# Kernel optimization log

Hardware: AMD Instinct MI355X
Metric: run time of the kernel (lower is better)

The kernel has to match this reference:

```python
import jax, jax.numpy as jnp
import numpy as np

B, M, T, H = 32, 2048, 8, 64  # batch, measurements, num_tags, hidden_dim
LATENT, TRIL = 3, 6
NEG_INF = -1e9  # masked-out logit value for segment softmax


def _linear_init(key, fan_in, fan_out):
    # torch nn.Linear default: U(-1/sqrt(fan_in), 1/sqrt(fan_in)) for W and b
    bound = 1.0 / np.sqrt(fan_in)
    kw, kb = jax.random.split(key)
    w = jax.random.uniform(kw, (fan_in, fan_out), minval=-bound, maxval=bound, dtype=jnp.float32)
    b = jax.random.uniform(kb, (fan_out,), minval=-bound, maxval=bound, dtype=jnp.float32)
    return w, b


def setup_inputs() -> dict:
    key = jax.random.key(0)
    ks = jax.random.split(key, 14)
    inp = {}
    inp['measurements'] = jax.random.normal(ks[0], (B, M, 5), dtype=jnp.float32)
    inp['measurement_to_tag_mapping'] = jax.random.randint(ks[1], (B, M), 0, T, dtype=jnp.int32)
    inp['me_w1'], inp['me_b1'] = _linear_init(ks[2], 5, H)
    inp['me_w2'], inp['me_b2'] = _linear_init(ks[3], H, H)
    inp['q_w'], inp['q_b'] = _linear_init(ks[4], H, H)
    inp['k_w'], inp['k_b'] = _linear_init(ks[5], H, H)
    inp['v_w'], inp['v_b'] = _linear_init(ks[6], H, H)
    inp['a1_w1'], inp['a1_b1'] = _linear_init(ks[7], H, H // 2)
    inp['a1_w2'], inp['a1_b2'] = _linear_init(ks[8], H // 2, 1)
    inp['a2_w1'], inp['a2_b1'] = _linear_init(ks[9], H, H // 2)
    inp['a2_w2'], inp['a2_b2'] = _linear_init(ks[10], H // 2, 1)
    inp['mu_w'], inp['mu_b'] = _linear_init(ks[11], H, LATENT)
    inp['logL_w'], inp['logL_b'] = _linear_init(ks[12], H, TRIL)
    return inp


def reference(measurements, measurement_to_tag_mapping,
              me_w1, me_b1, me_w2, me_b2,
              q_w, q_b, k_w, k_b, v_w, v_b,
              a1_w1, a1_b1, a1_w2, a1_b2,
              a2_w1, a2_b1, a2_w2, a2_b2,
              mu_w, mu_b, logL_w, logL_b):
    # measurement encoder: two Linear+ReLU layers -> [B, M, H]
    feat = jax.nn.relu(measurements @ me_w1 + me_b1)
    feat = jax.nn.relu(feat @ me_w2 + me_b2)

    # self-attention with residual
    q = feat @ q_w + q_b
    k = feat @ k_w + k_b
    v = feat @ v_w + v_b
    scale = jnp.sqrt(jnp.float32(H))
    scores = jnp.einsum('bmh,bnh->bmn', q, k) / scale  # [B, M, M]
    feat = feat + jnp.einsum('bmn,bnh->bmh', jax.nn.softmax(scores, axis=-1), v)

    # per-measurement attention logits (attention_net1) -> [B, M]
    a1 = (jax.nn.relu(feat @ a1_w1 + a1_b1) @ a1_w2 + a1_b2)[..., 0]

    # segment softmax per tag id: mask [B, M, T]
    tag_mask = measurement_to_tag_mapping[..., None] == jnp.arange(T)
    seg_logits = jnp.where(tag_mask, a1[..., None], NEG_INF)
    seg_w = jax.nn.softmax(seg_logits, axis=1)  # softmax over measurements within each tag
    tag_feat = jnp.einsum('bmt,bmh->bth', seg_w, feat)  # [B, T, H]

    # aggregate tags (attention_net2) -> pose feature [B, H]
    a2 = (jax.nn.relu(tag_feat @ a2_w1 + a2_b1) @ a2_w2 + a2_b2)[..., 0]  # [B, T]
    tag_w = jax.nn.softmax(a2, axis=-1)
    pose = jnp.einsum('bt,bth->bh', tag_w, tag_feat)

    mu = pose @ mu_w + mu_b
    logL = pose @ logL_w + logL_b
    return mu, logL
```

## Files before the change

kernel.cpp:

```cpp
#include <hip/hip_runtime.h>
#include <hip/hip_bf16.h>
#include <cstdint>
#include <cstddef>


typedef short s16x8 __attribute__((ext_vector_type(8)));
typedef float f32x4 __attribute__((ext_vector_type(4)));
typedef float f32x16 __attribute__((ext_vector_type(16)));

#define LOG2E  1.4426950408889634f
#define QSCALE 0.18033688011112042f

__device__ __forceinline__ unsigned short f2bf(float f) {
    unsigned u = __builtin_bit_cast(unsigned, f);
    u += 0x7fffu + ((u >> 16) & 1u);
    return (unsigned short)(u >> 16);
}

__device__ __forceinline__ unsigned cvtpk(float lo, float hi) {
    unsigned r;
    asm("v_cvt_pk_bf16_f32 %0, %1, %2" : "=v"(r) : "v"(lo), "v"(hi));
    return r;
}

__device__ __forceinline__ float exp2_raw(float x) {
    float r;
    asm("v_exp_f32 %0, %1" : "=v"(r) : "v"(x));
    return r;
}

#define PLSWAP(a, b) asm("v_permlane32_swap_b32 %0, %1" : "+v"(a), "+v"(b))

__device__ __forceinline__ void gload_lds16(const void* g, void* l) {
    __builtin_amdgcn_global_load_lds((const __attribute__((address_space(1))) void*)g,
                                     (__attribute__((address_space(3))) void*)l, 16, 0, 0);
}

#define MFMA16(a, b, c) __builtin_amdgcn_mfma_f32_16x16x32_bf16((a), (b), (c), 0, 0, 0)
#define MFMA32(a, b, c) __builtin_amdgcn_mfma_f32_32x32x16_bf16((a), (b), (c), 0, 0, 0)

__global__ void k_prep(const float* __restrict__ w2, const float* __restrict__ qw,
                       const float* __restrict__ kw, const float* __restrict__ vw,
                       const float* __restrict__ a1w1,
                       unsigned short* __restrict__ wt, float* __restrict__ a1w1t)
{
    int tid = threadIdx.x;
    for (int idx = tid; idx < 4096; idx += 256) {
        int o = idx >> 6, i = idx & 63;
        wt[idx]         = f2bf(w2[i * 64 + o]);
        wt[4096 + idx]  = f2bf(qw[i * 64 + o] * QSCALE);
        wt[8192 + idx]  = f2bf(kw[i * 64 + o]);
        wt[12288 + idx] = f2bf(vw[i * 64 + o]);
    }
    for (int idx = tid; idx < 2048; idx += 256) {
        int j = idx >> 6, d = idx & 63;
        a1w1t[idx] = a1w1[d * 32 + j];
    }
}

__global__ __launch_bounds__(256)
void k_encode(const float* __restrict__ meas, const float* __restrict__ w1,
              const float* __restrict__ b1, const float* __restrict__ b2,
              const float* __restrict__ qb, const float* __restrict__ kb,
              const float* __restrict__ vb,
              const unsigned short* __restrict__ wt,
              float* __restrict__ feat,
              unsigned short* __restrict__ qbf, unsigned short* __restrict__ kbf,
              unsigned short* __restrict__ vt)
{
    __shared__ __align__(16) unsigned short hbuf[4][1152];
    int tid = threadIdx.x;
    int w = tid >> 6, lane = tid & 63;
    int g = lane >> 4, c16 = lane & 15;
    int m0 = (blockIdx.x * 4 + w) * 16;
    int b  = m0 >> 11;
    unsigned short* hb = hbuf[w];
    int vrow = lane >> 2, vseg = lane & 3;

    float x[5];
    const float* xr = meas + (size_t)(m0 + c16) * 5;
#pragma unroll
    for (int i = 0; i < 5; ++i) x[i] = xr[i];
    s16x8 aH[2];
#pragma unroll
    for (int s = 0; s < 2; ++s) {
#pragma unroll
        for (int jj = 0; jj < 8; ++jj) {
            int j = 8 * g + jj + 32 * s;
            float acc = b1[j];
#pragma unroll
            for (int i = 0; i < 5; ++i) acc += x[i] * w1[i * 64 + j];
            aH[s][jj] = (short)f2bf(fmaxf(acc, 0.f));
        }
    }

    const f32x4 zero = {0.f, 0.f, 0.f, 0.f};
    f32x4 c[4];

#pragma unroll
    for (int dt = 0; dt < 4; ++dt) {
        c[dt] = zero;
#pragma unroll
        for (int s = 0; s < 2; ++s) {
            s16x8 bf = *(const s16x8*)(wt + (c16 + 16 * dt) * 64 + 32 * s + 8 * g);
            c[dt] = MFMA16(aH[s], bf, c[dt]);
        }
    }
#pragma unroll
    for (int dt = 0; dt < 4; ++dt) {
        int d = c16 + 16 * dt;
        float bias = b2[d];
#pragma unroll
        for (int r = 0; r < 4; ++r) {
            float v = fmaxf(c[dt][r] + bias, 0.f);
            feat[(size_t)(m0 + 4 * g + r) * 64 + d] = v;
            hb[(4 * g + r) * 72 + d] = f2bf(v);
        }
    }
    s16x8 aF[2];
#pragma unroll
    for (int s = 0; s < 2; ++s)
        aF[s] = *(const s16x8*)(hb + c16 * 72 + 32 * s + 8 * g);

    auto gemmW = [&](const unsigned short* wmat, f32x4* cc) {
#pragma unroll
        for (int dt = 0; dt < 4; ++dt) {
            cc[dt] = zero;
#pragma unroll
            for (int s = 0; s < 2; ++s) {
                s16x8 bf = *(const s16x8*)(wmat + (c16 + 16 * dt) * 64 + 32 * s + 8 * g);
                cc[dt] = MFMA16(aF[s], bf, cc[dt]);
            }
        }
    };
    auto storeV = [&](const float* bias4, unsigned short* dstbase) {
#pragma unroll
        for (int dt = 0; dt < 4; ++dt) {
            int d = c16 + 16 * dt;
#pragma unroll
            for (int r = 0; r < 4; ++r)
                hb[(4 * g + r) * 72 + d] = f2bf(c[dt][r] + bias4[dt]);
        }
        s16x8 o0 = *(const s16x8*)(hb + vrow * 72 + vseg * 16);
        s16x8 o1 = *(const s16x8*)(hb + vrow * 72 + vseg * 16 + 8);
        unsigned short* dst = dstbase + (size_t)(m0 + vrow) * 64 + vseg * 16;
        *(s16x8*)dst = o0;
        *(s16x8*)(dst + 8) = o1;
    };

    float bias4[4];
    gemmW(wt + 4096, c);
#pragma unroll
    for (int dt = 0; dt < 4; ++dt) bias4[dt] = qb[c16 + 16 * dt] * QSCALE;
    storeV(bias4, qbf);
    gemmW(wt + 8192, c);
#pragma unroll
    for (int dt = 0; dt < 4; ++dt) bias4[dt] = kb[c16 + 16 * dt];
    storeV(bias4, kbf);
    gemmW(wt + 12288, c);
#pragma unroll
    for (int dt = 0; dt < 4; ++dt) {
        int d = c16 + 16 * dt;
        float bias = vb[d];
#pragma unroll
        for (int r = 0; r < 4; ++r)
            hb[(4 * g + r) * 72 + d] = f2bf(c[dt][r] + bias);
    }
    unsigned short tvv[16];
#pragma unroll
    for (int mr = 0; mr < 16; ++mr) tvv[mr] = hb[mr * 72 + lane];
    s16x8 v0, v1;
#pragma unroll
    for (int e2 = 0; e2 < 8; ++e2) { v0[e2] = (short)tvv[e2]; v1[e2] = (short)tvv[8 + e2]; }
    unsigned short* dst = vt + ((size_t)b * 64 + lane) * 2048 + (m0 & 2047);
    *(s16x8*)dst = v0;
    *(s16x8*)(dst + 8) = v1;
}

__global__ __launch_bounds__(512, 4)
void k_attn(const unsigned short* __restrict__ qbf, const unsigned short* __restrict__ kbf,
            const unsigned short* __restrict__ vt, float* __restrict__ feat)
{
    __shared__ __align__(16) char smem[37888];

    int tid = threadIdx.x;
    int w_ = tid >> 6, lane = tid & 63;
    int h = lane >> 5, c32 = lane & 31;
    int jhalf = w_ & 1, tile = w_ >> 1;
    int bid = (int)blockIdx.x;
    bid = (bid & 7) * 64 + (bid >> 3);
    int b = bid >> 4;
    int q0g = (bid & 15) * 128 + tile * 32;
    size_t rowbase = (size_t)b * 2048;

    const unsigned short* kbf_b = kbf + rowbase * 64;
    const unsigned short* vt_b  = vt + (size_t)b * 64 * 2048;

    s16x8 qf[4];
    {
        const unsigned short* qp = qbf + (rowbase + q0g + c32) * 64 + 8 * h;
#pragma unroll
        for (int st = 0; st < 4; ++st)
            qf[st] = *(const s16x8*)(qp + 16 * st);
    }

    f32x16 zero16;
#pragma unroll
    for (int i = 0; i < 16; ++i) zero16[i] = 0.f;

    f32x16 o[2];
#pragma unroll
    for (int dt = 0; dt < 2; ++dt)
#pragma unroll
        for (int i = 0; i < 16; ++i) o[dt][i] = 0.f;
    float ll = 0.f;

    int srow = 8 * w_ + (lane >> 3);
    int scol = (lane & 7) ^ (srow & 7);
    const unsigned short* gk0 = kbf_b + (size_t)srow * 64 + scol * 8;
    const unsigned short* gv0 = vt_b + (size_t)srow * 2048 + scol * 8;

    auto stage = [&](int kt, int buf) {
        gload_lds16(gk0 + (size_t)kt * 4096, smem + buf * 8192 + w_ * 1024);
        gload_lds16(gv0 + kt * 64, smem + 16384 + buf * 8192 + w_ * 1024);
    };

    stage(0, 0);
    __syncthreads();

    int swz = c32 & 7;
    int krow = 32 * jhalf + c32;

    for (int kt = 0; kt < 32; ++kt) {
        int cur = kt & 1;
        if (kt + 1 < 32) stage(kt + 1, cur ^ 1);

        const char* Kb = smem + cur * 8192;
        const char* Vb = smem + 16384 + cur * 8192;

        s16x8 kf[4], vf[2][2];
#pragma unroll
        for (int st = 0; st < 4; ++st)
            kf[st] = *(const s16x8*)(Kb + krow * 128 + (((2 * st + h) ^ swz) * 16));
#pragma unroll
        for (int ks = 0; ks < 2; ++ks)
#pragma unroll
            for (int dt = 0; dt < 2; ++dt)
                vf[ks][dt] = *(const s16x8*)(Vb + (32 * dt + c32) * 128 +
                                             (((4 * jhalf + 2 * ks + h) ^ swz) * 16));

        __builtin_amdgcn_s_setprio(1);
        f32x16 sc = MFMA32(kf[0], qf[0], zero16);
#pragma unroll
        for (int st = 1; st < 4; ++st)
            sc = MFMA32(kf[st], qf[st], sc);
        __builtin_amdgcn_s_setprio(0);

        float p[16];
#pragma unroll
        for (int i = 0; i < 16; ++i) p[i] = exp2_raw(sc[i]);

        float s;
        {
            float a0 = p[0] + p[1],  a1 = p[2] + p[3],  a2 = p[4] + p[5],  a3 = p[6] + p[7];
            float a4 = p[8] + p[9],  a5 = p[10] + p[11], a6 = p[12] + p[13], a7 = p[14] + p[15];
            float b0 = a0 + a1, b1 = a2 + a3, b2 = a4 + a5, b3 = a6 + a7;
            s = (b0 + b1) + (b2 + b3);
        }
        {
            float s1 = s, s2 = s;
            PLSWAP(s1, s2);
            s = s1 + s2;
        }
        ll += s;

        unsigned u[8];
#pragma unroll
        for (int k2 = 0; k2 < 8; ++k2) u[k2] = cvtpk(p[2 * k2], p[2 * k2 + 1]);

        __builtin_amdgcn_s_setprio(1);
#pragma unroll
        for (int ks = 0; ks < 2; ++ks) {
            unsigned a0 = u[4 * ks + 0], b0 = u[4 * ks + 2];
            unsigned a1 = u[4 * ks + 1], b1 = u[4 * ks + 3];
            PLSWAP(a0, b0);
            PLSWAP(a1, b1);
            union { unsigned uu[4]; s16x8 v; } pa;
            pa.uu[0] = a0; pa.uu[1] = a1; pa.uu[2] = b0; pa.uu[3] = b1;
#pragma unroll
            for (int dt = 0; dt < 2; ++dt)
                o[dt] = MFMA32(pa.v, vf[ks][dt], o[dt]);
        }
        __builtin_amdgcn_s_setprio(0);
        __syncthreads();
    }

    float* Om = (float*)smem;
    float* Ml = (float*)(smem + 36864);
    if (jhalf) {
#pragma unroll
        for (int dt = 0; dt < 2; ++dt)
#pragma unroll
            for (int rg = 0; rg < 4; ++rg) {
                f32x4 vv;
#pragma unroll
                for (int r = 0; r < 4; ++r) vv[r] = o[dt][4 * rg + r];
                *(f32x4*)&Om[(tile * 64 + 32 * dt + c32) * 36 + 8 * rg + 4 * h] = vv;
            }
        if (h == 0) Ml[tile * 32 + c32] = ll;
    }
    __syncthreads();
    if (!jhalf) {
        float l1 = Ml[tile * 32 + c32];
        float f = 1.f / (ll + l1);
        float fr[16];
#pragma unroll
        for (int r = 0; r < 16; ++r) {
            int qrow = (r & 3) + 8 * (r >> 2) + 4 * h;
            fr[r] = __shfl(f, qrow);
        }
#pragma unroll
        for (int dt = 0; dt < 2; ++dt)
#pragma unroll
            for (int rg = 0; rg < 4; ++rg) {
                f32x4 pv = *(const f32x4*)&Om[(tile * 64 + 32 * dt + c32) * 36 + 8 * rg + 4 * h];
#pragma unroll
                for (int r = 0; r < 4; ++r) {
                    int rr = 4 * rg + r;
                    int qrow = r + 8 * rg + 4 * h;
                    size_t fi = (rowbase + q0g + qrow) * 64 + 32 * dt + c32;
                    feat[fi] += (o[dt][rr] + pv[r]) * fr[rr];
                }
            }
    }
}

__global__ __launch_bounds__(256)
void k_a1(const float* __restrict__ feat, const float* __restrict__ w1t,
          const float* __restrict__ b1, const float* __restrict__ w2,
          const float* __restrict__ b2, float* __restrict__ a1)
{
    int m = blockIdx.x * 256 + threadIdx.x;
    const f32x4* fr = (const f32x4*)(feat + (size_t)m * 64);

    float acc[32];
#pragma unroll
    for (int j = 0; j < 32; ++j) acc[j] = b1[j];

#pragma unroll
    for (int kc = 0; kc < 16; ++kc) {
        f32x4 f = fr[kc];
#pragma unroll
        for (int ki = 0; ki < 4; ++ki) {
            float fk = f[ki];
            int k = kc * 4 + ki;
#pragma unroll
            for (int j = 0; j < 32; ++j)
                acc[j] = fmaf(fk, w1t[j * 64 + k], acc[j]);
        }
    }
    float s = b2[0];
#pragma unroll
    for (int j = 0; j < 32; ++j) s += fmaxf(acc[j], 0.f) * w2[j];
    a1[m] = s;
}

__global__ __launch_bounds__(256)
void k_seg(const float* __restrict__ a1, const int* __restrict__ map,
           float* __restrict__ segstats)
{
    __shared__ float wred[4][8];
    __shared__ float MXs[8];
    int b = blockIdx.x;
    int tid = threadIdx.x, lane = tid & 63, w = tid >> 6;
    const float* a1b = a1 + b * 2048;
    const int* mp = map + b * 2048;

    float mx[8];
#pragma unroll
    for (int t = 0; t < 8; ++t) mx[t] = -1e9f;
    for (int m = tid; m < 2048; m += 256) {
        float v = a1b[m];
        int tg = mp[m];
#pragma unroll
        for (int t = 0; t < 8; ++t)
            if (tg == t) mx[t] = fmaxf(mx[t], v);
    }
#pragma unroll
    for (int t = 0; t < 8; ++t) {
        float v = mx[t];
        v = fmaxf(v, __shfl_xor(v, 1));  v = fmaxf(v, __shfl_xor(v, 2));
        v = fmaxf(v, __shfl_xor(v, 4));  v = fmaxf(v, __shfl_xor(v, 8));
        v = fmaxf(v, __shfl_xor(v, 16)); v = fmaxf(v, __shfl_xor(v, 32));
        mx[t] = v;
    }
    if (lane == 0) {
#pragma unroll
        for (int t = 0; t < 8; ++t) wred[w][t] = mx[t];
    }
    __syncthreads();
    if (tid < 8) {
        float v = fmaxf(fmaxf(wred[0][tid], wred[1][tid]),
                        fmaxf(wred[2][tid], wred[3][tid]));
        MXs[tid] = v;
        segstats[b * 16 + tid] = v;
    }
    __syncthreads();

    float sm[8];
#pragma unroll
    for (int t = 0; t < 8; ++t) sm[t] = 0.f;
    for (int m = tid; m < 2048; m += 256) {
        float v = a1b[m];
        int tg = mp[m];
        float e = exp2f((v - MXs[tg]) * LOG2E);
#pragma unroll
        for (int t = 0; t < 8; ++t)
            if (tg == t) sm[t] += e;
    }
#pragma unroll
    for (int t = 0; t < 8; ++t) {
        float v = sm[t];
        v += __shfl_xor(v, 1);  v += __shfl_xor(v, 2);
        v += __shfl_xor(v, 4);  v += __shfl_xor(v, 8);
        v += __shfl_xor(v, 16); v += __shfl_xor(v, 32);
        sm[t] = v;
    }
    __syncthreads();
    if (lane == 0) {
#pragma unroll
        for (int t = 0; t < 8; ++t) wred[w][t] = sm[t];
    }
    __syncthreads();
    if (tid < 8)
        segstats[b * 16 + 8 + tid] =
            1.f / (wred[0][tid] + wred[1][tid] + wred[2][tid] + wred[3][tid]);
}

__global__ __launch_bounds__(256)
void k_tagfeat(const float* __restrict__ a1, const int* __restrict__ map,
               const float* __restrict__ feat, const float* __restrict__ segstats,
               float* __restrict__ part)
{
    __shared__ float accv[4][8][64];
    __shared__ float MXs[8], SMIs[8];
    int b = blockIdx.x >> 4;
    int c = blockIdx.x & 15;
    int tid = threadIdx.x, lane = tid & 63, w = tid >> 6;

    if (tid < 16) {
        float v = segstats[b * 16 + tid];
        if (tid < 8) MXs[tid] = v; else SMIs[tid - 8] = v;
    }
    __syncthreads();

    const float* a1b = a1 + b * 2048;
    const int* mp = map + b * 2048;
    int m0 = c * 128;

    float tacc[8];
#pragma unroll
    for (int t = 0; t < 8; ++t) tacc[t] = 0.f;
    for (int mi = w; mi < 128; mi += 4) {
        int m = m0 + mi;
        float v = a1b[m];
        int tg = mp[m];
        float wgt = exp2f((v - MXs[tg]) * LOG2E) * SMIs[tg];
        float wf = wgt * feat[((size_t)b * 2048 + m) * 64 + lane];
#pragma unroll
        for (int t = 0; t < 8; ++t)
            if (tg == t) tacc[t] += wf;
    }
#pragma unroll
    for (int t = 0; t < 8; ++t) accv[w][t][lane] = tacc[t];
    __syncthreads();
    for (int e = tid; e < 512; e += 256) {
        int t = e >> 6, d = e & 63;
        part[((size_t)c * 32 + b) * 512 + e] =
            accv[0][t][d] + accv[1][t][d] + accv[2][t][d] + accv[3][t][d];
    }
}

__global__ __launch_bounds__(256)
void k_head(const float* __restrict__ part,
            const float* __restrict__ a2w1, const float* __restrict__ a2b1,
            const float* __restrict__ a2w2, const float* __restrict__ a2b2,
            const float* __restrict__ muw, const float* __restrict__ mub,
            const float* __restrict__ lLw, const float* __restrict__ lLb,
            float* __restrict__ out)
{
    __shared__ float tf[8][64];
    __shared__ float sc8[8];
    __shared__ float pose[64];
    int b = blockIdx.x;
    int tid = threadIdx.x;

    for (int e = tid; e < 512; e += 256) {
        float s = 0.f;
#pragma unroll
        for (int c = 0; c < 16; ++c) s += part[((size_t)c * 32 + b) * 512 + e];
        tf[e >> 6][e & 63] = s;
    }
    __syncthreads();

    {
        int t = tid >> 5, j = tid & 31;
        float acc = a2b1[j];
        for (int d = 0; d < 64; ++d) acc += tf[t][d] * a2w1[d * 32 + j];
        float hsum = fmaxf(acc, 0.f) * a2w2[j];
        hsum += __shfl_xor(hsum, 1);
        hsum += __shfl_xor(hsum, 2);
        hsum += __shfl_xor(hsum, 4);
        hsum += __shfl_xor(hsum, 8);
        hsum += __shfl_xor(hsum, 16);
        if (j == 0) sc8[t] = hsum + a2b2[0];
    }
    __syncthreads();
    if (tid < 64) {
        float smax = sc8[0];
#pragma unroll
        for (int t = 1; t < 8; ++t) smax = fmaxf(smax, sc8[t]);
        float e[8], ssum = 0.f;
#pragma unroll
        for (int t = 0; t < 8; ++t) { e[t] = exp2f((sc8[t] - smax) * LOG2E); ssum += e[t]; }
        float rinv = 1.f / ssum;
        float p = 0.f;
#pragma unroll
        for (int t = 0; t < 8; ++t) p += (e[t] * rinv) * tf[t][tid];
        pose[tid] = p;
    }
    __syncthreads();
    if (tid < 3) {
        float acc = mub[tid];
        for (int d = 0; d < 64; ++d) acc += pose[d] * muw[d * 3 + tid];
        out[b * 3 + tid] = acc;
    }
    if (tid >= 32 && tid < 38) {
        int oo = tid - 32;
        float acc = lLb[oo];
        for (int d = 0; d < 64; ++d) acc += pose[d] * lLw[d * 6 + oo];
        out[96 + b * 6 + oo] = acc;
    }
}

extern "C" void kernel_launch(void* const* d_in, const int* in_sizes, int n_in,
                              void* d_out, int out_size, void* d_ws, size_t ws_size,
                              hipStream_t stream)
{
    (void)in_sizes; (void)n_in; (void)out_size; (void)ws_size;

    const float* measurements = (const float*)d_in[0];
    const int*   mapping      = (const int*)d_in[1];
    const float* me_w1 = (const float*)d_in[2];
    const float* me_b1 = (const float*)d_in[3];
    const float* me_w2 = (const float*)d_in[4];
    const float* me_b2 = (const float*)d_in[5];
    const float* q_w   = (const float*)d_in[6];
    const float* q_b   = (const float*)d_in[7];
    const float* k_w   = (const float*)d_in[8];
    const float* k_b   = (const float*)d_in[9];
    const float* v_w   = (const float*)d_in[10];
    const float* v_b   = (const float*)d_in[11];
    const float* a1_w1 = (const float*)d_in[12];
    const float* a1_b1 = (const float*)d_in[13];
    const float* a1_w2 = (const float*)d_in[14];
    const float* a1_b2 = (const float*)d_in[15];
    const float* a2_w1 = (const float*)d_in[16];
    const float* a2_b1 = (const float*)d_in[17];
    const float* a2_w2 = (const float*)d_in[18];
    const float* a2_b2 = (const float*)d_in[19];
    const float* mu_w  = (const float*)d_in[20];
    const float* mu_b  = (const float*)d_in[21];
    const float* logL_w = (const float*)d_in[22];
    const float* logL_b = (const float*)d_in[23];

    char* ws = (char*)d_ws;
    unsigned short* wt    = (unsigned short*)(ws);
    float*          a1w1t = (float*)(ws + 32768);
    float*          feat  = (float*)(ws + 40960);
    unsigned short* qbf   = (unsigned short*)(ws + 16818176);
    unsigned short* kbf   = (unsigned short*)(ws + 25206784);
    unsigned short* vt    = (unsigned short*)(ws + 33595392);
    float*          a1    = (float*)(ws + 41984000);
    float*          segst = (float*)(ws + 42246144);
    float*          part  = (float*)(ws + 42248192);
    float*          out   = (float*)d_out;

    k_prep<<<1, 256, 0, stream>>>(me_w2, q_w, k_w, v_w, a1_w1, wt, a1w1t);
    k_encode<<<1024, 256, 0, stream>>>(measurements, me_w1, me_b1, me_b2, q_b, k_b, v_b,
                                       wt, feat, qbf, kbf, vt);
    k_attn<<<512, 512, 0, stream>>>(qbf, kbf, vt, feat);
    k_a1<<<256, 256, 0, stream>>>(feat, a1w1t, a1_b1, a1_w2, a1_b2, a1);
    k_seg<<<32, 256, 0, stream>>>(a1, mapping, segst);
    k_tagfeat<<<512, 256, 0, stream>>>(a1, mapping, feat, segst, part);
    k_head<<<32, 256, 0, stream>>>(part, a2_w1, a2_b1, a2_w2, a2_b2,
                                   mu_w, mu_b, logL_w, logL_b, out);
}
```

Baseline: 124.7 us.

## Fuse a1 logits, segment softmax and tag aggregation into one kernel

Merges k_a1, k_seg and k_tagfeat into a single kernel. Each block computes the a1 logits for its 128 rows, splitting K across two thread halves, then accumulates exp-weighted features and per-tag exp sums as partials. The max subtraction is dropped and the normalisation moves into k_head. This removes two launches and the a1 and segstats round trips, and k_prep is spread over 8 blocks. The price is possible overflow or underflow in the unnormalised exp if logits are large.

```diff
diff --git a/kernel.cpp b/kernel.cpp
--- a/kernel.cpp
+++ b/kernel.cpp
@@ -41,20 +41,15 @@
 
 __global__ void k_prep(const float* __restrict__ w2, const float* __restrict__ qw,
                        const float* __restrict__ kw, const float* __restrict__ vw,
-                       const float* __restrict__ a1w1,
-                       unsigned short* __restrict__ wt, float* __restrict__ a1w1t)
+                       unsigned short* __restrict__ wt)
 {
-    int tid = threadIdx.x;
-    for (int idx = tid; idx < 4096; idx += 256) {
+    int tid = blockIdx.x * 256 + threadIdx.x;
+    for (int idx = tid; idx < 4096; idx += 2048) {
         int o = idx >> 6, i = idx & 63;
         wt[idx]         = f2bf(w2[i * 64 + o]);
         wt[4096 + idx]  = f2bf(qw[i * 64 + o] * QSCALE);
         wt[8192 + idx]  = f2bf(kw[i * 64 + o]);
         wt[12288 + idx] = f2bf(vw[i * 64 + o]);
-    }
-    for (int idx = tid; idx < 2048; idx += 256) {
-        int j = idx >> 6, d = idx & 63;
-        a1w1t[idx] = a1w1[d * 32 + j];
     }
 }
 
@@ -336,153 +331,82 @@
 }
 
 __global__ __launch_bounds__(256)
-void k_a1(const float* __restrict__ feat, const float* __restrict__ w1t,
-          const float* __restrict__ b1, const float* __restrict__ w2,
-          const float* __restrict__ b2, float* __restrict__ a1)
+void k_a1tag(const float* __restrict__ feat, const int* __restrict__ map,
+             const float* __restrict__ a1w1, const float* __restrict__ b1,
+             const float* __restrict__ w2, const float* __restrict__ b2,
+             float* __restrict__ part1, float* __restrict__ part0)
 {
-    int m = blockIdx.x * 256 + threadIdx.x;
-    const f32x4* fr = (const f32x4*)(feat + (size_t)m * 64);
-
-    float acc[32];
-#pragma unroll
-    for (int j = 0; j < 32; ++j) acc[j] = b1[j];
-
-#pragma unroll
-    for (int kc = 0; kc < 16; ++kc) {
-        f32x4 f = fr[kc];
-#pragma unroll
-        for (int ki = 0; ki < 4; ++ki) {
-            float fk = f[ki];
-            int k = kc * 4 + ki;
-#pragma unroll
-            for (int j = 0; j < 32; ++j)
-                acc[j] = fmaf(fk, w1t[j * 64 + k], acc[j]);
-        }
-    }
-    float s = b2[0];
-#pragma unroll
-    for (int j = 0; j < 32; ++j) s += fmaxf(acc[j], 0.f) * w2[j];
-    a1[m] = s;
-}
-
-__global__ __launch_bounds__(256)
-void k_seg(const float* __restrict__ a1, const int* __restrict__ map,
-           float* __restrict__ segstats)
-{
-    __shared__ float wred[4][8];
-    __shared__ float MXs[8];
-    int b = blockIdx.x;
-    int tid = threadIdx.x, lane = tid & 63, w = tid >> 6;
-    const float* a1b = a1 + b * 2048;
-    const int* mp = map + b * 2048;
-
-    float mx[8];
-#pragma unroll
-    for (int t = 0; t < 8; ++t) mx[t] = -1e9f;
-    for (int m = tid; m < 2048; m += 256) {
-        float v = a1b[m];
-        int tg = mp[m];
-#pragma unroll
-        for (int t = 0; t < 8; ++t)
-            if (tg == t) mx[t] = fmaxf(mx[t], v);
-    }
-#pragma unroll
-    for (int t = 0; t < 8; ++t) {
-        float v = mx[t];
-        v = fmaxf(v, __shfl_xor(v, 1));  v = fmaxf(v, __shfl_xor(v, 2));
-        v = fmaxf(v, __shfl_xor(v, 4));  v = fmaxf(v, __shfl_xor(v, 8));
-        v = fmaxf(v, __shfl_xor(v, 16)); v = fmaxf(v, __shfl_xor(v, 32));
-        mx[t] = v;
-    }
-    if (lane == 0) {
-#pragma unroll
-        for (int t = 0; t < 8; ++t) wred[w][t] = mx[t];
-    }
-    __syncthreads();
-    if (tid < 8) {
-        float v = fmaxf(fmaxf(wred[0][tid], wred[1][tid]),
-                        fmaxf(wred[2][tid], wred[3][tid]));
-        MXs[tid] = v;
-        segstats[b * 16 + tid] = v;
-    }
-    __syncthreads();
-
-    float sm[8];
-#pragma unroll
-    for (int t = 0; t < 8; ++t) sm[t] = 0.f;
-    for (int m = tid; m < 2048; m += 256) {
-        float v = a1b[m];
-        int tg = mp[m];
-        float e = exp2f((v - MXs[tg]) * LOG2E);
-#pragma unroll
-        for (int t = 0; t < 8; ++t)
-            if (tg == t) sm[t] += e;
-    }
-#pragma unroll
-    for (int t = 0; t < 8; ++t) {
-        float v = sm[t];
-        v += __shfl_xor(v, 1);  v += __shfl_xor(v, 2);
-        v += __shfl_xor(v, 4);  v += __shfl_xor(v, 8);
-        v += __shfl_xor(v, 16); v += __shfl_xor(v, 32);
-        sm[t] = v;
-    }
-    __syncthreads();
-    if (lane == 0) {
-#pragma unroll
-        for (int t = 0; t < 8; ++t) wred[w][t] = sm[t];
-    }
-    __syncthreads();
-    if (tid < 8)
-        segstats[b * 16 + 8 + tid] =
-            1.f / (wred[0][tid] + wred[1][tid] + wred[2][tid] + wred[3][tid]);
-}
-
-__global__ __launch_bounds__(256)
-void k_tagfeat(const float* __restrict__ a1, const int* __restrict__ map,
-               const float* __restrict__ feat, const float* __restrict__ segstats,
-               float* __restrict__ part)
-{
+    __shared__ float psum[128][33];
+    __shared__ float es[128];
     __shared__ float accv[4][8][64];
-    __shared__ float MXs[8], SMIs[8];
+    __shared__ float s0red[4][8];
+
     int b = blockIdx.x >> 4;
     int c = blockIdx.x & 15;
     int tid = threadIdx.x, lane = tid & 63, w = tid >> 6;
-
-    if (tid < 16) {
-        float v = segstats[b * 16 + tid];
-        if (tid < 8) MXs[tid] = v; else SMIs[tid - 8] = v;
-    }
-    __syncthreads();
-
-    const float* a1b = a1 + b * 2048;
-    const int* mp = map + b * 2048;
     int m0 = c * 128;
-
-    float tacc[8];
-#pragma unroll
-    for (int t = 0; t < 8; ++t) tacc[t] = 0.f;
+    const int* mp = map + b * 2048 + m0;
+    const float* fbase = feat + ((size_t)b * 2048 + m0) * 64;
+
+    {
+        int r = tid & 127, kh = tid >> 7;
+        const float* fr = fbase + (size_t)r * 64 + kh * 32;
+        float acc[32];
+#pragma unroll
+        for (int j = 0; j < 32; ++j) acc[j] = kh ? 0.f : b1[j];
+#pragma unroll
+        for (int kk = 0; kk < 32; ++kk) {
+            float fv = fr[kk];
+            const float* wr = a1w1 + (kh * 32 + kk) * 32;
+#pragma unroll
+            for (int j = 0; j < 32; ++j)
+                acc[j] = fmaf(fv, wr[j], acc[j]);
+        }
+        if (kh) {
+#pragma unroll
+            for (int j = 0; j < 32; ++j) psum[r][j] = acc[j];
+        }
+        __syncthreads();
+        if (!kh) {
+            float s = b2[0];
+#pragma unroll
+            for (int j = 0; j < 32; ++j)
+                s += fmaxf(acc[j] + psum[r][j], 0.f) * w2[j];
+            es[r] = exp2_raw(s * LOG2E);
+        }
+    }
+    __syncthreads();
+
+    float tacc[8], s0t[8];
+#pragma unroll
+    for (int t = 0; t < 8; ++t) { tacc[t] = 0.f; s0t[t] = 0.f; }
     for (int mi = w; mi < 128; mi += 4) {
-        int m = m0 + mi;
-        float v = a1b[m];
-        int tg = mp[m];
-        float wgt = exp2f((v - MXs[tg]) * LOG2E) * SMIs[tg];
-        float wf = wgt * feat[((size_t)b * 2048 + m) * 64 + lane];
+        int tg = mp[mi];
+        float e = es[mi];
+        float wf = e * fbase[(size_t)mi * 64 + lane];
 #pragma unroll
         for (int t = 0; t < 8; ++t)
-            if (tg == t) tacc[t] += wf;
+            if (tg == t) { tacc[t] += wf; s0t[t] += e; }
     }
 #pragma unroll
     for (int t = 0; t < 8; ++t) accv[w][t][lane] = tacc[t];
+    if (lane == 0) {
+#pragma unroll
+        for (int t = 0; t < 8; ++t) s0red[w][t] = s0t[t];
+    }
     __syncthreads();
     for (int e = tid; e < 512; e += 256) {
         int t = e >> 6, d = e & 63;
-        part[((size_t)c * 32 + b) * 512 + e] =
+        part1[((size_t)c * 32 + b) * 512 + e] =
             accv[0][t][d] + accv[1][t][d] + accv[2][t][d] + accv[3][t][d];
     }
+    if (tid < 8)
+        part0[((size_t)c * 32 + b) * 8 + tid] =
+            s0red[0][tid] + s0red[1][tid] + s0red[2][tid] + s0red[3][tid];
 }
 
 __global__ __launch_bounds__(256)
-void k_head(const float* __restrict__ part,
+void k_head(const float* __restrict__ part1, const float* __restrict__ part0,
             const float* __restrict__ a2w1, const float* __restrict__ a2b1,
             const float* __restrict__ a2w2, const float* __restrict__ a2b2,
             const float* __restrict__ muw, const float* __restrict__ mub,
@@ -490,16 +414,24 @@
             float* __restrict__ out)
 {
     __shared__ float tf[8][64];
+    __shared__ float deni[8];
     __shared__ float sc8[8];
     __shared__ float pose[64];
     int b = blockIdx.x;
     int tid = threadIdx.x;
 
+    if (tid < 8) {
+        float s = 0.f;
+#pragma unroll
+        for (int c = 0; c < 16; ++c) s += part0[((size_t)c * 32 + b) * 8 + tid];
+        deni[tid] = 1.f / s;
+    }
+    __syncthreads();
     for (int e = tid; e < 512; e += 256) {
         float s = 0.f;
 #pragma unroll
-        for (int c = 0; c < 16; ++c) s += part[((size_t)c * 32 + b) * 512 + e];
-        tf[e >> 6][e & 63] = s;
+        for (int c = 0; c < 16; ++c) s += part1[((size_t)c * 32 + b) * 512 + e];
+        tf[e >> 6][e & 63] = s * deni[e >> 6];
     }
     __syncthreads();
 
@@ -576,23 +508,20 @@
 
     char* ws = (char*)d_ws;
     unsigned short* wt    = (unsigned short*)(ws);
-    float*          a1w1t = (float*)(ws + 32768);
     float*          feat  = (float*)(ws + 40960);
     unsigned short* qbf   = (unsigned short*)(ws + 16818176);
     unsigned short* kbf   = (unsigned short*)(ws + 25206784);
     unsigned short* vt    = (unsigned short*)(ws + 33595392);
-    float*          a1    = (float*)(ws + 41984000);
-    float*          segst = (float*)(ws + 42246144);
-    float*          part  = (float*)(ws + 42248192);
+    float*          part1 = (float*)(ws + 42248192);
+    float*          part0 = (float*)(ws + 43296768);
     float*          out   = (float*)d_out;
 
-    k_prep<<<1, 256, 0, stream>>>(me_w2, q_w, k_w, v_w, a1_w1, wt, a1w1t);
+    k_prep<<<8, 256, 0, stream>>>(me_w2, q_w, k_w, v_w, wt);
     k_encode<<<1024, 256, 0, stream>>>(measurements, me_w1, me_b1, me_b2, q_b, k_b, v_b,
                                        wt, feat, qbf, kbf, vt);
     k_attn<<<512, 512, 0, stream>>>(qbf, kbf, vt, feat);
-    k_a1<<<256, 256, 0, stream>>>(feat, a1w1t, a1_b1, a1_w2, a1_b2, a1);
-    k_seg<<<32, 256, 0, stream>>>(a1, mapping, segst);
-    k_tagfeat<<<512, 256, 0, stream>>>(a1, mapping, feat, segst, part);
-    k_head<<<32, 256, 0, stream>>>(part, a2_w1, a2_b1, a2_w2, a2_b2,
+    k_a1tag<<<512, 256, 0, stream>>>(feat, mapping, a1_w1, a1_b1, a1_w2, a1_b2,
+                                     part1, part0);
+    k_head<<<32, 256, 0, stream>>>(part1, part0, a2_w1, a2_b1, a2_w2, a2_b2,
                                    mu_w, mu_b, logL_w, logL_b, out);
 }
```

New measurement: 110.8 us. -11.2%, faster.
